# Kernel tuning notes

Hardware: AMD Instinct MI355X
Metric: run time of the kernel (lower is better)

Reference implementation:

```python
import jax, jax.numpy as jnp
import numpy as np

B, C, H, E, K, QT = 256, 1024, 64, 64, 2, 20000

def _mlp(x, W1, b1, W2, b2):
    # GKT MLP (eval mode: dropout off; batch-norm omitted, see notes)
    return jax.nn.relu(jax.nn.relu(x @ W1 + b1) @ W2 + b2)

def setup_inputs() -> dict:
    key = jax.random.key(0)
    ks = jax.random.split(key, 30)
    s = 0.05  # weight scale to keep pre-clamp activations in a sane range
    xt = jax.random.uniform(ks[0], (B,), dtype=jnp.float32)
    qt = jax.random.randint(ks[1], (B,), 0, QT)
    ht = jax.random.normal(ks[2], (B, C, H), dtype=jnp.float32)
    # binary question->concept incidence, ~4 KCs per question, col 0 forced on
    oh = (jax.random.uniform(ks[3], (QT, C)) < 4.0 / C).astype(jnp.float32)
    oh = oh.at[:, 0].set(1.0)
    qt_kc_one_hot = jnp.concatenate([oh, jnp.zeros((1, C), jnp.float32)], axis=0)  # zero padding row
    kc_embeddings = jax.random.normal(ks[4], (C, E), dtype=jnp.float32) * 0.1
    graphs = jax.random.uniform(ks[5], (K, C, C), dtype=jnp.float32)  # graph_model output
    neigh_weight = jnp.float32(0.8)
    MI = H + E
    Ws1 = jax.random.normal(ks[6], (MI, H), jnp.float32) * s; bs1 = jnp.zeros((H,), jnp.float32)
    Ws2 = jax.random.normal(ks[7], (H, H), jnp.float32) * s;  bs2 = jnp.zeros((H,), jnp.float32)
    Wn1 = jax.random.normal(ks[8], (K, 2 * MI, H), jnp.float32) * s; bn1 = jnp.zeros((K, H), jnp.float32)
    Wn2 = jax.random.normal(ks[9], (K, H, H), jnp.float32) * s;      bn2 = jnp.zeros((K, H), jnp.float32)
    ea_w = jax.random.uniform(ks[10], (C,), dtype=jnp.float32)
    We = jax.random.normal(ks[11], (H, H), jnp.float32) * s; be = jnp.zeros((H,), jnp.float32)
    Wa = jax.random.normal(ks[12], (H, H), jnp.float32) * s; ba = jnp.zeros((H,), jnp.float32)
    W_ih = jax.random.normal(ks[13], (H, 3 * H), jnp.float32) * s; b_ih = jnp.zeros((3 * H,), jnp.float32)
    W_hh = jax.random.normal(ks[14], (H, 3 * H), jnp.float32) * s; b_hh = jnp.zeros((3 * H,), jnp.float32)
    Wp = jax.random.normal(ks[15], (H, 1), jnp.float32) * s; bp = jnp.zeros((1,), jnp.float32)
    return dict(xt=xt, qt=qt, ht=ht, qt_kc_one_hot=qt_kc_one_hot, kc_embeddings=kc_embeddings,
                graphs=graphs, neigh_weight=neigh_weight, Ws1=Ws1, bs1=bs1, Ws2=Ws2, bs2=bs2,
                Wn1=Wn1, bn1=bn1, Wn2=Wn2, bn2=bn2, ea_w=ea_w, We=We, be=be, Wa=Wa, ba=ba,
                W_ih=W_ih, b_ih=b_ih, W_hh=W_hh, b_hh=b_hh, Wp=Wp, bp=bp)

def reference(xt, qt, ht, qt_kc_one_hot, kc_embeddings, graphs, neigh_weight,
              Ws1, bs1, Ws2, bs2, Wn1, bn1, Wn2, bn2, ea_w, We, be, Wa, ba,
              W_ih, b_ih, W_hh, b_hh, Wp, bp):
    # ---- _aggregate: the fusion loops never write back, so tmp_ht = cat(ht, kc_emb)
    mask = qt_kc_one_hot[qt]                                   # [B, C] gather of binary incidence
    kc = jnp.broadcast_to(kc_embeddings[None], (mask.shape[0], C, E))
    tmp_ht = jnp.concatenate([ht, kc], axis=-1)                # [B, C, H+E]
    # ---- _agg_neighbors
    self_ht = tmp_ht * mask[..., None]
    self_feat = jnp.clip(_mlp(self_ht, Ws1, bs1, Ws2, bs2), -10.0, 10.0)
    neigh_ht = jnp.clip(jnp.concatenate([self_ht, tmp_ht], axis=-1), -5.0, 5.0)  # [B,C,2(H+E)]
    # bug-faithful adj: mean of graphs[k] rows over sample 0's active concepts
    a0 = mask[0]                                               # [C]
    denom = jnp.maximum(a0.sum(), 1.0)
    adj = jnp.clip(jnp.einsum('c,kcd->kd', a0, graphs) / denom, -5.0, 5.0)       # [K, C]
    nb = jax.vmap(lambda W1, b1, W2, b2: _mlp(neigh_ht, W1, b1, W2, b2))(Wn1, bn1, Wn2, bn2)
    nb = jnp.clip(nb, -5.0, 5.0)                               # [K, B, C, H]
    w = jnp.clip(neigh_weight, 0.1, 0.9)
    nf = jnp.clip(adj[0][None, :, None] * nb[0], -5.0, 5.0)
    for k in range(1, K):
        nf = jnp.clip(w * nf + (1.0 - w) * adj[k][None, :, None] * nb[k], -5.0, 5.0)
    m_next = jnp.clip(jnp.where(mask[..., None] > 0.5, self_feat, nf), -50.0, 50.0)
    # ---- erase-add gate
    g = ea_w[None, :, None]
    res = m_next - g * jax.nn.sigmoid(m_next @ We + be) * m_next + g * jnp.tanh(m_next @ Wa + ba)
    # ---- GRUCell over flattened (B*C) rows
    gi = res @ W_ih + b_ih
    gh = ht @ W_hh + b_hh
    ir, iz, in_ = jnp.split(gi, 3, axis=-1)
    hr, hz, hn = jnp.split(gh, 3, axis=-1)
    r = jax.nn.sigmoid(ir + hr)
    z = jax.nn.sigmoid(iz + hz)
    n = jnp.tanh(in_ + r * hn)
    h_next = (1.0 - z) * n + z * ht                            # [B, C, H]
    y = jax.nn.sigmoid(h_next @ Wp + bp)[..., 0]               # [B, C]
    return y
```

## Files before the change

### kernel.cpp

```cpp
#include <hip/hip_runtime.h>

#define DEVINL __device__ __forceinline__

typedef __bf16 bf16x8 __attribute__((ext_vector_type(8)));
typedef float  f32x4  __attribute__((ext_vector_type(4)));

static constexpr size_t kAdjOff  = 0;
static constexpr size_t kBiasOff = 8192;
static constexpr size_t kFragOff = 8192 + 786432;

static constexpr int FB_Wn1h0 = 0,  FB_Wn1h1 = 8,  FB_Wn2_0 = 16, FB_Wn2_1 = 24;
static constexpr int FB_Ws1h  = 32, FB_Ws2   = 40, FB_We    = 48, FB_Wa    = 56;
static constexpr int FB_Wih   = 64, FB_Whh   = 88;

DEVINL unsigned short bf16r(float f) {
  unsigned u = __builtin_bit_cast(unsigned, f);
  unsigned r = ((u >> 16) & 1u) + 0x7FFFu;
  return (unsigned short)((u + r) >> 16);
}
DEVINL float sigmoidf_(float x) { return __builtin_amdgcn_rcpf(1.f + __expf(-x)); }
DEVINL float tanhf_(float x)    { return 1.f - 2.f * __builtin_amdgcn_rcpf(1.f + __expf(2.f * x)); }

DEVINL void lds_fence() {
  __builtin_amdgcn_sched_barrier(0);
  __builtin_amdgcn_s_waitcnt(0xC07F);
  __builtin_amdgcn_sched_barrier(0);
}

DEVINL f32x4 mfma16(bf16x8 a, bf16x8 b, f32x4 c) {
  return __builtin_amdgcn_mfma_f32_16x16x32_bf16(a, b, c, 0, 0, 0);
}

DEVINL unsigned clip2_(unsigned x) {
  float lo = __builtin_bit_cast(float, x << 16);
  float hi = __builtin_bit_cast(float, x & 0xFFFF0000u);
  lo = fminf(fmaxf(lo, -5.f), 5.f);
  hi = fminf(fmaxf(hi, -5.f), 5.f);
  return (__builtin_bit_cast(unsigned, lo) >> 16) | (__builtin_bit_cast(unsigned, hi) & 0xFFFF0000u);
}
DEVINL bf16x8 clip5(bf16x8 a) {
  uint4 u = __builtin_bit_cast(uint4, a);
  u.x = clip2_(u.x); u.y = clip2_(u.y); u.z = clip2_(u.z); u.w = clip2_(u.w);
  return __builtin_bit_cast(bf16x8, u);
}

__global__ void prep_adj_kernel(const int* __restrict__ qt, const float* __restrict__ onehot,
                                const float* __restrict__ graphs, float* __restrict__ adjw) {
  __shared__ float a0[1024];
  __shared__ float s_denom;
  const int tid = threadIdx.x;
  const int k = blockIdx.x >> 2, chunk = blockIdx.x & 3;
  const int q0 = qt[0];
  for (int i = tid; i < 1024; i += 256) a0[i] = onehot[(size_t)q0 * 1024 + i];
  __syncthreads();
  if (tid < 64) {
    float s = 0.f;
#pragma unroll
    for (int i = 0; i < 16; i++) s += a0[tid * 16 + i];
#pragma unroll
    for (int off = 32; off >= 1; off >>= 1) s += __shfl_xor(s, off, 64);
    if (tid == 0) s_denom = fmaxf(s, 1.0f);
  }
  __syncthreads();
  const int d = chunk * 256 + tid;
  const float* G = graphs + (size_t)k * 1024 * 1024 + d;
  float sum = 0.f;
  for (int c = 0; c < 1024; c++) sum += a0[c] * G[(size_t)c * 1024];
  adjw[k * 1024 + d] = fminf(fmaxf(sum / s_denom, -5.f), 5.f);
}

__global__ void prep_bias_kernel(const float* __restrict__ kc, const float* __restrict__ Wn1,
                                 const float* __restrict__ bn1, const float* __restrict__ Ws1,
                                 const float* __restrict__ bs1, float* __restrict__ biasTab) {
  int gid = blockIdx.x * 256 + threadIdx.x;
  int j = gid & 63;
  int c = (gid >> 6) & 1023;
  int tab = gid >> 16;
  const float* kcr = kc + (size_t)c * 64;
  float s;
  if (tab < 2) {
    s = bn1[tab * 64 + j];
    const float* W = Wn1 + ((size_t)tab * 256 + 192) * 64 + j;
#pragma unroll 4
    for (int e = 0; e < 64; e++) s += fminf(fmaxf(kcr[e], -5.f), 5.f) * W[(size_t)e * 64];
  } else {
    s = bs1[j];
    const float* W = Ws1 + (size_t)64 * 64 + j;
#pragma unroll 4
    for (int e = 0; e < 64; e++) s += kcr[e] * W[(size_t)e * 64];
  }
  int c16 = c >> 4, rr = c & 3, qq = (c & 15) >> 2, nt = j >> 4;
  int lane = qq * 16 + (j & 15);
  biasTab[(size_t)((((c16 * 3 + tab) * 4 + nt) * 64 + lane)) * 4 + rr] = s;
}

__global__ void prep_wfrag_kernel(const float* __restrict__ Wn1, const float* __restrict__ Wn2,
                                  const float* __restrict__ Ws1, const float* __restrict__ Ws2,
                                  const float* __restrict__ We,  const float* __restrict__ Wa,
                                  const float* __restrict__ Wih, const float* __restrict__ Whh,
                                  uint4* __restrict__ wfrag) {
  const int bid = blockIdx.x, lane = threadIdx.x;
  int mat, ks, nt;
  if (bid < 64) { mat = bid >> 3; ks = (bid >> 2) & 1; nt = bid & 3; }
  else { int f2 = bid - 64; mat = 8 + f2 / 24; int f = f2 % 24; ks = f / 12; nt = f % 12; }
  const float* base = Wn1; int stride = 64;
  switch (mat) {
    case 0: base = Wn1 + (size_t)128 * 64; break;
    case 1: base = Wn1 + (size_t)(256 + 128) * 64; break;
    case 2: base = Wn2; break;
    case 3: base = Wn2 + (size_t)64 * 64; break;
    case 4: base = Ws1; break;
    case 5: base = Ws2; break;
    case 6: base = We; break;
    case 7: base = Wa; break;
    case 8: base = Wih; stride = 192; break;
    case 9: base = Whh; stride = 192; break;
  }
  const int qq = lane >> 4, col = nt * 16 + (lane & 15);
  union { unsigned short u[8]; uint4 v; } tmp;
#pragma unroll
  for (int jj = 0; jj < 8; jj++) {
    int k = ks * 32 + qq * 8 + jj;
    tmp.u[jj] = bf16r(base[(size_t)k * stride + col]);
  }
  wfrag[(size_t)bid * 64 + lane] = tmp.v;
}

__global__ __launch_bounds__(256, 2) void gkt_main_kernel(
    const int* __restrict__ qt, const float* __restrict__ onehot, const float* __restrict__ ht,
    const float* __restrict__ nw, const float* __restrict__ bn2, const float* __restrict__ be,
    const float* __restrict__ ba, const float* __restrict__ bih, const float* __restrict__ bhh,
    const float* __restrict__ Wp, const float* __restrict__ bp, const float* __restrict__ eaw,
    const float* __restrict__ bs2, const float* __restrict__ adjw, const float* __restrict__ biasTab,
    const bf16x8* __restrict__ wfrag, float* __restrict__ out) {
  __shared__ __align__(16) unsigned short xbuf[4][32][72];
  __shared__ __align__(16) unsigned short hbuf[4][32][72];
  __shared__ float tokp[4][128];

  const int tid = threadIdx.x;
  const int wv = tid >> 6, lane = tid & 63;
  const int q = lane >> 4, cl = lane & 15;
  const int t0 = (blockIdx.x * 4 + wv) * 32;
  const int b = t0 >> 10, c0 = t0 & 1023, c16 = c0 >> 4;

  unsigned short* xb = &xbuf[wv][0][0];
  unsigned short* hb = &hbuf[wv][0][0];
  float* tp = &tokp[wv][0];

  if (lane < 32) {
    const int c = c0 + lane;
    tp[lane]      = onehot[(size_t)qt[b] * 1024 + c];
    tp[32 + lane] = adjw[c];
    tp[64 + lane] = adjw[1024 + c];
    tp[96 + lane] = eaw[c];
  }
  {
    const float4* ht4 = (const float4*)ht;
#pragma unroll
    for (int i = 0; i < 8; i++) {
      float4 v = ht4[(size_t)t0 * 16 + i * 64 + lane];
      int e = i * 64 + lane;
      int tok = e >> 4, coll = (e & 15) * 4;
      ushort4 h;
      h.x = bf16r(v.x); h.y = bf16r(v.y); h.z = bf16r(v.z); h.w = bf16r(v.w);
      *(ushort4*)&xbuf[wv][tok][coll] = h;
    }
  }
  lds_fence();

  const float wmix = fminf(fmaxf(nw[0], 0.1f), 0.9f);
  float wp4[4];
#pragma unroll
  for (int nt = 0; nt < 4; nt++) wp4[nt] = Wp[nt * 16 + cl];
  const float bpv = bp[0];

  auto ldA = [&](const unsigned short* buf, int mt, int ks) -> bf16x8 {
    return *(const bf16x8*)(buf + (cl + 16 * mt) * 72 + ks * 32 + q * 8);
  };
  auto ldB = [&](int frag) -> bf16x8 { return wfrag[frag * 64 + lane]; };
  const f32x4* bt4 = (const f32x4*)biasTab;

  bf16x8 xc[2][2];
#pragma unroll
  for (int mt = 0; mt < 2; mt++)
#pragma unroll
    for (int ks = 0; ks < 2; ks++) xc[mt][ks] = clip5(ldA(xb, mt, ks));

  f32x4 nf[2][4];
#pragma unroll
  for (int k2 = 0; k2 < 2; k2++) {
    f32x4 acc[2][4];
#pragma unroll
    for (int mt = 0; mt < 2; mt++)
#pragma unroll
      for (int nt = 0; nt < 4; nt++)
        acc[mt][nt] = bt4[(((c16 + mt) * 3 + k2) * 4 + nt) * 64 + lane];
#pragma unroll
    for (int ks = 0; ks < 2; ks++)
#pragma unroll
      for (int nt = 0; nt < 4; nt++) {
        bf16x8 bb = ldB((k2 ? FB_Wn1h1 : FB_Wn1h0) + ks * 4 + nt);
        acc[0][nt] = mfma16(xc[0][ks], bb, acc[0][nt]);
        acc[1][nt] = mfma16(xc[1][ks], bb, acc[1][nt]);
      }
    lds_fence();
#pragma unroll
    for (int mt = 0; mt < 2; mt++)
#pragma unroll
      for (int nt = 0; nt < 4; nt++)
#pragma unroll
        for (int r = 0; r < 4; r++)
          hb[(16 * mt + q * 4 + r) * 72 + nt * 16 + cl] = bf16r(fmaxf(acc[mt][nt][r], 0.f));
    lds_fence();
    f32x4 acc2[2][4];
#pragma unroll
    for (int nt = 0; nt < 4; nt++) {
      float bz = bn2[k2 * 64 + nt * 16 + cl];
      f32x4 iv = {bz, bz, bz, bz};
      acc2[0][nt] = iv; acc2[1][nt] = iv;
    }
#pragma unroll
    for (int ks = 0; ks < 2; ks++) {
      bf16x8 a0 = ldA(hb, 0, ks), a1 = ldA(hb, 1, ks);
#pragma unroll
      for (int nt = 0; nt < 4; nt++) {
        bf16x8 bb = ldB((k2 ? FB_Wn2_1 : FB_Wn2_0) + ks * 4 + nt);
        acc2[0][nt] = mfma16(a0, bb, acc2[0][nt]);
        acc2[1][nt] = mfma16(a1, bb, acc2[1][nt]);
      }
    }
#pragma unroll
    for (int mt = 0; mt < 2; mt++)
#pragma unroll
      for (int nt = 0; nt < 4; nt++)
#pragma unroll
        for (int r = 0; r < 4; r++) {
          int tok = 16 * mt + q * 4 + r;
          float nb = fminf(fmaxf(acc2[mt][nt][r], 0.f), 5.f);
          float v = tp[(1 + k2) * 32 + tok] * nb;
          if (k2 == 0) nf[mt][nt][r] = wmix * fminf(fmaxf(v, -5.f), 5.f);
          else         nf[mt][nt][r] = fminf(fmaxf(nf[mt][nt][r] + (1.f - wmix) * v, -5.f), 5.f);
        }
  }

  bool anySelf = __any((lane < 32) && (tp[lane] > 0.5f));
  if (anySelf) {
    bf16x8 xr[2][2];
#pragma unroll
    for (int mt = 0; mt < 2; mt++)
#pragma unroll
      for (int ks = 0; ks < 2; ks++) xr[mt][ks] = ldA(xb, mt, ks);
    f32x4 acc[2][4];
#pragma unroll
    for (int mt = 0; mt < 2; mt++)
#pragma unroll
      for (int nt = 0; nt < 4; nt++)
        acc[mt][nt] = bt4[(((c16 + mt) * 3 + 2) * 4 + nt) * 64 + lane];
#pragma unroll
    for (int ks = 0; ks < 2; ks++)
#pragma unroll
      for (int nt = 0; nt < 4; nt++) {
        bf16x8 bb = ldB(FB_Ws1h + ks * 4 + nt);
        acc[0][nt] = mfma16(xr[0][ks], bb, acc[0][nt]);
        acc[1][nt] = mfma16(xr[1][ks], bb, acc[1][nt]);
      }
    lds_fence();
#pragma unroll
    for (int mt = 0; mt < 2; mt++)
#pragma unroll
      for (int nt = 0; nt < 4; nt++)
#pragma unroll
        for (int r = 0; r < 4; r++)
          hb[(16 * mt + q * 4 + r) * 72 + nt * 16 + cl] = bf16r(fmaxf(acc[mt][nt][r], 0.f));
    lds_fence();
    f32x4 acc2[2][4];
#pragma unroll
    for (int nt = 0; nt < 4; nt++) {
      float bz = bs2[nt * 16 + cl];
      f32x4 iv = {bz, bz, bz, bz};
      acc2[0][nt] = iv; acc2[1][nt] = iv;
    }
#pragma unroll
    for (int ks = 0; ks < 2; ks++) {
      bf16x8 a0 = ldA(hb, 0, ks), a1 = ldA(hb, 1, ks);
#pragma unroll
      for (int nt = 0; nt < 4; nt++) {
        bf16x8 bb = ldB(FB_Ws2 + ks * 4 + nt);
        acc2[0][nt] = mfma16(a0, bb, acc2[0][nt]);
        acc2[1][nt] = mfma16(a1, bb, acc2[1][nt]);
      }
    }
#pragma unroll
    for (int mt = 0; mt < 2; mt++)
#pragma unroll
      for (int nt = 0; nt < 4; nt++)
#pragma unroll
        for (int r = 0; r < 4; r++) {
          int tok = 16 * mt + q * 4 + r;
          float sf = fminf(fmaxf(acc2[mt][nt][r], 0.f), 10.f);
          nf[mt][nt][r] = (tp[tok] > 0.5f) ? sf : nf[mt][nt][r];
        }
  }

  lds_fence();
#pragma unroll
  for (int mt = 0; mt < 2; mt++)
#pragma unroll
    for (int nt = 0; nt < 4; nt++)
#pragma unroll
      for (int r = 0; r < 4; r++)
        hb[(16 * mt + q * 4 + r) * 72 + nt * 16 + cl] = bf16r(nf[mt][nt][r]);
  lds_fence();
  bf16x8 mf[2][2];
#pragma unroll
  for (int mt = 0; mt < 2; mt++)
#pragma unroll
    for (int ks = 0; ks < 2; ks++) mf[mt][ks] = ldA(hb, mt, ks);
  {
    f32x4 accE[2][4];
#pragma unroll
    for (int nt = 0; nt < 4; nt++) {
      float bz = be[nt * 16 + cl];
      f32x4 iv = {bz, bz, bz, bz};
      accE[0][nt] = iv; accE[1][nt] = iv;
    }
#pragma unroll
    for (int ks = 0; ks < 2; ks++)
#pragma unroll
      for (int nt = 0; nt < 4; nt++) {
        bf16x8 bb = ldB(FB_We + ks * 4 + nt);
        accE[0][nt] = mfma16(mf[0][ks], bb, accE[0][nt]);
        accE[1][nt] = mfma16(mf[1][ks], bb, accE[1][nt]);
      }
#pragma unroll
    for (int mt = 0; mt < 2; mt++)
#pragma unroll
      for (int nt = 0; nt < 4; nt++)
#pragma unroll
        for (int r = 0; r < 4; r++) {
          int tok = 16 * mt + q * 4 + r;
          float g = tp[96 + tok];
          float m = nf[mt][nt][r];
          nf[mt][nt][r] = m - g * sigmoidf_(accE[mt][nt][r]) * m;
        }
    f32x4 accA[2][4];
#pragma unroll
    for (int nt = 0; nt < 4; nt++) {
      float bz = ba[nt * 16 + cl];
      f32x4 iv = {bz, bz, bz, bz};
      accA[0][nt] = iv; accA[1][nt] = iv;
    }
#pragma unroll
    for (int ks = 0; ks < 2; ks++)
#pragma unroll
      for (int nt = 0; nt < 4; nt++) {
        bf16x8 bb = ldB(FB_Wa + ks * 4 + nt);
        accA[0][nt] = mfma16(mf[0][ks], bb, accA[0][nt]);
        accA[1][nt] = mfma16(mf[1][ks], bb, accA[1][nt]);
      }
#pragma unroll
    for (int mt = 0; mt < 2; mt++)
#pragma unroll
      for (int nt = 0; nt < 4; nt++)
#pragma unroll
        for (int r = 0; r < 4; r++) {
          int tok = 16 * mt + q * 4 + r;
          nf[mt][nt][r] += tp[96 + tok] * tanhf_(accA[mt][nt][r]);
        }
  }

  lds_fence();
#pragma unroll
  for (int mt = 0; mt < 2; mt++)
#pragma unroll
    for (int nt = 0; nt < 4; nt++)
#pragma unroll
      for (int r = 0; r < 4; r++)
        hb[(16 * mt + q * 4 + r) * 72 + nt * 16 + cl] = bf16r(nf[mt][nt][r]);
  lds_fence();
  bf16x8 rf[2][2], xr2[2][2];
#pragma unroll
  for (int mt = 0; mt < 2; mt++)
#pragma unroll
    for (int ks = 0; ks < 2; ks++) { rf[mt][ks] = ldA(hb, mt, ks); xr2[mt][ks] = ldA(xb, mt, ks); }

  f32x4 gR[2][4], gZ[2][4], gN[2][4], gH[2][4];
#pragma unroll
  for (int nt = 0; nt < 4; nt++) {
    int col = nt * 16 + cl;
    float brz = bih[col] + bhh[col];
    float bzz = bih[64 + col] + bhh[64 + col];
    float bnn = bih[128 + col];
    float bhn = bhh[128 + col];
    f32x4 v;
    v = {brz, brz, brz, brz}; gR[0][nt] = v; gR[1][nt] = v;
    v = {bzz, bzz, bzz, bzz}; gZ[0][nt] = v; gZ[1][nt] = v;
    v = {bnn, bnn, bnn, bnn}; gN[0][nt] = v; gN[1][nt] = v;
    v = {bhn, bhn, bhn, bhn}; gH[0][nt] = v; gH[1][nt] = v;
  }
#pragma unroll
  for (int ks = 0; ks < 2; ks++)
#pragma unroll
    for (int nt = 0; nt < 4; nt++) {
      bf16x8 bi_r = ldB(FB_Wih + ks * 12 + nt);
      bf16x8 bh_r = ldB(FB_Whh + ks * 12 + nt);
      bf16x8 bi_z = ldB(FB_Wih + ks * 12 + 4 + nt);
      bf16x8 bh_z = ldB(FB_Whh + ks * 12 + 4 + nt);
      bf16x8 bi_n = ldB(FB_Wih + ks * 12 + 8 + nt);
      bf16x8 bh_n = ldB(FB_Whh + ks * 12 + 8 + nt);
#pragma unroll
      for (int mt = 0; mt < 2; mt++) {
        gR[mt][nt] = mfma16(rf[mt][ks],  bi_r, gR[mt][nt]);
        gR[mt][nt] = mfma16(xr2[mt][ks], bh_r, gR[mt][nt]);
        gZ[mt][nt] = mfma16(rf[mt][ks],  bi_z, gZ[mt][nt]);
        gZ[mt][nt] = mfma16(xr2[mt][ks], bh_z, gZ[mt][nt]);
        gN[mt][nt] = mfma16(rf[mt][ks],  bi_n, gN[mt][nt]);
        gH[mt][nt] = mfma16(xr2[mt][ks], bh_n, gH[mt][nt]);
      }
    }
#pragma unroll
  for (int mt = 0; mt < 2; mt++)
#pragma unroll
    for (int nt = 0; nt < 4; nt++)
#pragma unroll
      for (int r = 0; r < 4; r++) {
        gR[mt][nt][r] = sigmoidf_(gR[mt][nt][r]);
        gZ[mt][nt][r] = sigmoidf_(gZ[mt][nt][r]);
      }

#pragma unroll
  for (int mt = 0; mt < 2; mt++)
#pragma unroll
    for (int r = 0; r < 4; r++) {
      int tok = 16 * mt + q * 4 + r;
      float part = 0.f;
#pragma unroll
      for (int nt = 0; nt < 4; nt++) {
        float nval = tanhf_(gN[mt][nt][r] + gR[mt][nt][r] * gH[mt][nt][r]);
        float z = gZ[mt][nt][r];
        float htv = ht[(size_t)(t0 + tok) * 64 + nt * 16 + cl];
        float hnx = (1.f - z) * nval + z * htv;
        part += hnx * wp4[nt];
      }
      part += __shfl_xor(part, 1, 64);
      part += __shfl_xor(part, 2, 64);
      part += __shfl_xor(part, 4, 64);
      part += __shfl_xor(part, 8, 64);
      if (cl == 0) out[t0 + tok] = sigmoidf_(part + bpv);
    }
}

extern "C" void kernel_launch(void* const* d_in, const int* in_sizes, int n_in,
                              void* d_out, int out_size, void* d_ws, size_t ws_size,
                              hipStream_t stream) {
  const int*   qt     = (const int*)d_in[1];
  const float* ht     = (const float*)d_in[2];
  const float* onehot = (const float*)d_in[3];
  const float* kc     = (const float*)d_in[4];
  const float* graphs = (const float*)d_in[5];
  const float* nw     = (const float*)d_in[6];
  const float* Ws1    = (const float*)d_in[7];
  const float* bs1    = (const float*)d_in[8];
  const float* Ws2    = (const float*)d_in[9];
  const float* bs2    = (const float*)d_in[10];
  const float* Wn1    = (const float*)d_in[11];
  const float* bn1    = (const float*)d_in[12];
  const float* Wn2    = (const float*)d_in[13];
  const float* bn2    = (const float*)d_in[14];
  const float* eaw    = (const float*)d_in[15];
  const float* We     = (const float*)d_in[16];
  const float* be     = (const float*)d_in[17];
  const float* Wa     = (const float*)d_in[18];
  const float* ba     = (const float*)d_in[19];
  const float* Wih    = (const float*)d_in[20];
  const float* bih    = (const float*)d_in[21];
  const float* Whh    = (const float*)d_in[22];
  const float* bhh    = (const float*)d_in[23];
  const float* Wp     = (const float*)d_in[24];
  const float* bp     = (const float*)d_in[25];
  float* out = (float*)d_out;

  float* adjw    = (float*)((char*)d_ws + kAdjOff);
  float* biasTab = (float*)((char*)d_ws + kBiasOff);
  uint4* wfragU  = (uint4*)((char*)d_ws + kFragOff);

  prep_adj_kernel<<<8, 256, 0, stream>>>(qt, onehot, graphs, adjw);
  prep_bias_kernel<<<768, 256, 0, stream>>>(kc, Wn1, bn1, Ws1, bs1, biasTab);
  prep_wfrag_kernel<<<112, 64, 0, stream>>>(Wn1, Wn2, Ws1, Ws2, We, Wa, Wih, Whh, wfragU);
  gkt_main_kernel<<<2048, 256, 0, stream>>>(qt, onehot, ht, nw, bn2, be, ba, bih, bhh,
                                            Wp, bp, eaw, bs2, adjw, biasTab,
                                            (const bf16x8*)wfragU, out);
}
```

Baseline: 314.4 us.

## Drop xbuf LDS, keep ht in registers, raise occupancy, sparsify adj prep

The main kernel stops keeping a separate LDS buffer for ht. It loads the ht fragments once into registers and reuses them for the self-MLP and the GRU hidden matmul. The freed LDS and the launch bounds raised to 4 blocks per CU aim at higher occupancy, and the per-token scalars are now read as vector loads. The adjacency prep now gathers only the nonzero one-hot entries (about 4 of 1024), which removes nearly all of its strided graph reads. The risks are register spilling under the tighter occupancy target and extra live registers for xr.

```diff
diff --git a/kernel.cpp b/kernel.cpp
--- a/kernel.cpp
+++ b/kernel.cpp
@@ -46,27 +46,34 @@
 
 __global__ void prep_adj_kernel(const int* __restrict__ qt, const float* __restrict__ onehot,
                                 const float* __restrict__ graphs, float* __restrict__ adjw) {
-  __shared__ float a0[1024];
-  __shared__ float s_denom;
+  __shared__ float a0v[1024];
+  __shared__ int   aidx[1024];
+  __shared__ int   s_nnz;
+  __shared__ float s_den;
   const int tid = threadIdx.x;
   const int k = blockIdx.x >> 2, chunk = blockIdx.x & 3;
+  if (tid == 0) { s_nnz = 0; s_den = 0.f; }
+  __syncthreads();
   const int q0 = qt[0];
-  for (int i = tid; i < 1024; i += 256) a0[i] = onehot[(size_t)q0 * 1024 + i];
+  float lsum = 0.f;
+#pragma unroll
+  for (int i = 0; i < 4; i++) {
+    int c = tid * 4 + i;
+    float v = onehot[(size_t)q0 * 1024 + c];
+    lsum += v;
+    if (v != 0.f) { int p = atomicAdd(&s_nnz, 1); aidx[p] = c; a0v[p] = v; }
+  }
+#pragma unroll
+  for (int off = 32; off >= 1; off >>= 1) lsum += __shfl_xor(lsum, off, 64);
+  if ((tid & 63) == 0) atomicAdd(&s_den, lsum);
   __syncthreads();
-  if (tid < 64) {
-    float s = 0.f;
-#pragma unroll
-    for (int i = 0; i < 16; i++) s += a0[tid * 16 + i];
-#pragma unroll
-    for (int off = 32; off >= 1; off >>= 1) s += __shfl_xor(s, off, 64);
-    if (tid == 0) s_denom = fmaxf(s, 1.0f);
-  }
-  __syncthreads();
+  const float denom = fmaxf(s_den, 1.f);
+  const int nnz = s_nnz;
   const int d = chunk * 256 + tid;
-  const float* G = graphs + (size_t)k * 1024 * 1024 + d;
+  const float* G = graphs + (size_t)k * 1048576 + d;
   float sum = 0.f;
-  for (int c = 0; c < 1024; c++) sum += a0[c] * G[(size_t)c * 1024];
-  adjw[k * 1024 + d] = fminf(fmaxf(sum / s_denom, -5.f), 5.f);
+  for (int j = 0; j < nnz; j++) sum += a0v[j] * G[(size_t)aidx[j] * 1024];
+  adjw[k * 1024 + d] = fminf(fmaxf(sum / denom, -5.f), 5.f);
 }
 
 __global__ void prep_bias_kernel(const float* __restrict__ kc, const float* __restrict__ Wn1,
@@ -126,16 +133,15 @@
   wfrag[(size_t)bid * 64 + lane] = tmp.v;
 }
 
-__global__ __launch_bounds__(256, 2) void gkt_main_kernel(
+__global__ __launch_bounds__(256, 4) void gkt_main_kernel(
     const int* __restrict__ qt, const float* __restrict__ onehot, const float* __restrict__ ht,
     const float* __restrict__ nw, const float* __restrict__ bn2, const float* __restrict__ be,
     const float* __restrict__ ba, const float* __restrict__ bih, const float* __restrict__ bhh,
     const float* __restrict__ Wp, const float* __restrict__ bp, const float* __restrict__ eaw,
     const float* __restrict__ bs2, const float* __restrict__ adjw, const float* __restrict__ biasTab,
     const bf16x8* __restrict__ wfrag, float* __restrict__ out) {
-  __shared__ __align__(16) unsigned short xbuf[4][32][72];
   __shared__ __align__(16) unsigned short hbuf[4][32][72];
-  __shared__ float tokp[4][128];
+  __shared__ __align__(16) float tokp[4][128];
 
   const int tid = threadIdx.x;
   const int wv = tid >> 6, lane = tid & 63;
@@ -143,7 +149,6 @@
   const int t0 = (blockIdx.x * 4 + wv) * 32;
   const int b = t0 >> 10, c0 = t0 & 1023, c16 = c0 >> 4;
 
-  unsigned short* xb = &xbuf[wv][0][0];
   unsigned short* hb = &hbuf[wv][0][0];
   float* tp = &tokp[wv][0];
 
@@ -163,7 +168,7 @@
       int tok = e >> 4, coll = (e & 15) * 4;
       ushort4 h;
       h.x = bf16r(v.x); h.y = bf16r(v.y); h.z = bf16r(v.z); h.w = bf16r(v.w);
-      *(ushort4*)&xbuf[wv][tok][coll] = h;
+      *(ushort4*)&hbuf[wv][tok][coll] = h;
     }
   }
   lds_fence();
@@ -174,36 +179,104 @@
   for (int nt = 0; nt < 4; nt++) wp4[nt] = Wp[nt * 16 + cl];
   const float bpv = bp[0];
 
-  auto ldA = [&](const unsigned short* buf, int mt, int ks) -> bf16x8 {
-    return *(const bf16x8*)(buf + (cl + 16 * mt) * 72 + ks * 32 + q * 8);
+  auto ldA = [&](int mt, int ks) -> bf16x8 {
+    return *(const bf16x8*)(hb + (cl + 16 * mt) * 72 + ks * 32 + q * 8);
   };
   auto ldB = [&](int frag) -> bf16x8 { return wfrag[frag * 64 + lane]; };
+  auto ldTP4 = [&](int base, int mt) -> f32x4 {
+    return *(const f32x4*)(tp + base + 16 * mt + q * 4);
+  };
   const f32x4* bt4 = (const f32x4*)biasTab;
 
-  bf16x8 xc[2][2];
-#pragma unroll
-  for (int mt = 0; mt < 2; mt++)
-#pragma unroll
-    for (int ks = 0; ks < 2; ks++) xc[mt][ks] = clip5(ldA(xb, mt, ks));
+  bf16x8 xr[2][2];
+#pragma unroll
+  for (int mt = 0; mt < 2; mt++)
+#pragma unroll
+    for (int ks = 0; ks < 2; ks++) xr[mt][ks] = ldA(mt, ks);
+  lds_fence();
 
   f32x4 nf[2][4];
-#pragma unroll
-  for (int k2 = 0; k2 < 2; k2++) {
+  {
+    bf16x8 xc[2][2];
+#pragma unroll
+    for (int mt = 0; mt < 2; mt++)
+#pragma unroll
+      for (int ks = 0; ks < 2; ks++) xc[mt][ks] = clip5(xr[mt][ks]);
+
+#pragma unroll
+    for (int k2 = 0; k2 < 2; k2++) {
+      f32x4 acc[2][4];
+#pragma unroll
+      for (int mt = 0; mt < 2; mt++)
+#pragma unroll
+        for (int nt = 0; nt < 4; nt++)
+          acc[mt][nt] = bt4[(((c16 + mt) * 3 + k2) * 4 + nt) * 64 + lane];
+#pragma unroll
+      for (int ks = 0; ks < 2; ks++)
+#pragma unroll
+        for (int nt = 0; nt < 4; nt++) {
+          bf16x8 bb = ldB((k2 ? FB_Wn1h1 : FB_Wn1h0) + ks * 4 + nt);
+          acc[0][nt] = mfma16(xc[0][ks], bb, acc[0][nt]);
+          acc[1][nt] = mfma16(xc[1][ks], bb, acc[1][nt]);
+        }
+#pragma unroll
+      for (int mt = 0; mt < 2; mt++)
+#pragma unroll
+        for (int nt = 0; nt < 4; nt++)
+#pragma unroll
+          for (int r = 0; r < 4; r++)
+            hb[(16 * mt + q * 4 + r) * 72 + nt * 16 + cl] = bf16r(fmaxf(acc[mt][nt][r], 0.f));
+      lds_fence();
+      f32x4 acc2[2][4];
+#pragma unroll
+      for (int nt = 0; nt < 4; nt++) {
+        float bz = bn2[k2 * 64 + nt * 16 + cl];
+        f32x4 iv = {bz, bz, bz, bz};
+        acc2[0][nt] = iv; acc2[1][nt] = iv;
+      }
+#pragma unroll
+      for (int ks = 0; ks < 2; ks++) {
+        bf16x8 a0 = ldA(0, ks), a1 = ldA(1, ks);
+#pragma unroll
+        for (int nt = 0; nt < 4; nt++) {
+          bf16x8 bb = ldB((k2 ? FB_Wn2_1 : FB_Wn2_0) + ks * 4 + nt);
+          acc2[0][nt] = mfma16(a0, bb, acc2[0][nt]);
+          acc2[1][nt] = mfma16(a1, bb, acc2[1][nt]);
+        }
+      }
+      lds_fence();
+#pragma unroll
+      for (int mt = 0; mt < 2; mt++) {
+        f32x4 adjv = ldTP4((1 + k2) * 32, mt);
+#pragma unroll
+        for (int nt = 0; nt < 4; nt++)
+#pragma unroll
+          for (int r = 0; r < 4; r++) {
+            float nb = fminf(fmaxf(acc2[mt][nt][r], 0.f), 5.f);
+            float v = adjv[r] * nb;
+            if (k2 == 0) nf[mt][nt][r] = wmix * fminf(fmaxf(v, -5.f), 5.f);
+            else         nf[mt][nt][r] = fminf(fmaxf(nf[mt][nt][r] + (1.f - wmix) * v, -5.f), 5.f);
+          }
+      }
+    }
+  }
+
+  bool anySelf = __any((lane < 32) && (tp[lane] > 0.5f));
+  if (anySelf) {
     f32x4 acc[2][4];
 #pragma unroll
     for (int mt = 0; mt < 2; mt++)
 #pragma unroll
       for (int nt = 0; nt < 4; nt++)
-        acc[mt][nt] = bt4[(((c16 + mt) * 3 + k2) * 4 + nt) * 64 + lane];
+        acc[mt][nt] = bt4[(((c16 + mt) * 3 + 2) * 4 + nt) * 64 + lane];
 #pragma unroll
     for (int ks = 0; ks < 2; ks++)
 #pragma unroll
       for (int nt = 0; nt < 4; nt++) {
-        bf16x8 bb = ldB((k2 ? FB_Wn1h1 : FB_Wn1h0) + ks * 4 + nt);
-        acc[0][nt] = mfma16(xc[0][ks], bb, acc[0][nt]);
-        acc[1][nt] = mfma16(xc[1][ks], bb, acc[1][nt]);
-      }
-    lds_fence();
+        bf16x8 bb = ldB(FB_Ws1h + ks * 4 + nt);
+        acc[0][nt] = mfma16(xr[0][ks], bb, acc[0][nt]);
+        acc[1][nt] = mfma16(xr[1][ks], bb, acc[1][nt]);
+      }
 #pragma unroll
     for (int mt = 0; mt < 2; mt++)
 #pragma unroll
@@ -215,74 +288,13 @@
     f32x4 acc2[2][4];
 #pragma unroll
     for (int nt = 0; nt < 4; nt++) {
-      float bz = bn2[k2 * 64 + nt * 16 + cl];
-      f32x4 iv = {bz, bz, bz, bz};
-      acc2[0][nt] = iv; acc2[1][nt] = iv;
-    }
-#pragma unroll
-    for (int ks = 0; ks < 2; ks++) {
-      bf16x8 a0 = ldA(hb, 0, ks), a1 = ldA(hb, 1, ks);
-#pragma unroll
-      for (int nt = 0; nt < 4; nt++) {
-        bf16x8 bb = ldB((k2 ? FB_Wn2_1 : FB_Wn2_0) + ks * 4 + nt);
-        acc2[0][nt] = mfma16(a0, bb, acc2[0][nt]);
-        acc2[1][nt] = mfma16(a1, bb, acc2[1][nt]);
-      }
-    }
-#pragma unroll
-    for (int mt = 0; mt < 2; mt++)
-#pragma unroll
-      for (int nt = 0; nt < 4; nt++)
-#pragma unroll
-        for (int r = 0; r < 4; r++) {
-          int tok = 16 * mt + q * 4 + r;
-          float nb = fminf(fmaxf(acc2[mt][nt][r], 0.f), 5.f);
-          float v = tp[(1 + k2) * 32 + tok] * nb;
-          if (k2 == 0) nf[mt][nt][r] = wmix * fminf(fmaxf(v, -5.f), 5.f);
-          else         nf[mt][nt][r] = fminf(fmaxf(nf[mt][nt][r] + (1.f - wmix) * v, -5.f), 5.f);
-        }
-  }
-
-  bool anySelf = __any((lane < 32) && (tp[lane] > 0.5f));
-  if (anySelf) {
-    bf16x8 xr[2][2];
-#pragma unroll
-    for (int mt = 0; mt < 2; mt++)
-#pragma unroll
-      for (int ks = 0; ks < 2; ks++) xr[mt][ks] = ldA(xb, mt, ks);
-    f32x4 acc[2][4];
-#pragma unroll
-    for (int mt = 0; mt < 2; mt++)
-#pragma unroll
-      for (int nt = 0; nt < 4; nt++)
-        acc[mt][nt] = bt4[(((c16 + mt) * 3 + 2) * 4 + nt) * 64 + lane];
-#pragma unroll
-    for (int ks = 0; ks < 2; ks++)
-#pragma unroll
-      for (int nt = 0; nt < 4; nt++) {
-        bf16x8 bb = ldB(FB_Ws1h + ks * 4 + nt);
-        acc[0][nt] = mfma16(xr[0][ks], bb, acc[0][nt]);
-        acc[1][nt] = mfma16(xr[1][ks], bb, acc[1][nt]);
-      }
-    lds_fence();
-#pragma unroll
-    for (int mt = 0; mt < 2; mt++)
-#pragma unroll
-      for (int nt = 0; nt < 4; nt++)
-#pragma unroll
-        for (int r = 0; r < 4; r++)
-          hb[(16 * mt + q * 4 + r) * 72 + nt * 16 + cl] = bf16r(fmaxf(acc[mt][nt][r], 0.f));
-    lds_fence();
-    f32x4 acc2[2][4];
-#pragma unroll
-    for (int nt = 0; nt < 4; nt++) {
       float bz = bs2[nt * 16 + cl];
       f32x4 iv = {bz, bz, bz, bz};
       acc2[0][nt] = iv; acc2[1][nt] = iv;
     }
 #pragma unroll
     for (int ks = 0; ks < 2; ks++) {
-      bf16x8 a0 = ldA(hb, 0, ks), a1 = ldA(hb, 1, ks);
+      bf16x8 a0 = ldA(0, ks), a1 = ldA(1, ks);
 #pragma unroll
       for (int nt = 0; nt < 4; nt++) {
         bf16x8 bb = ldB(FB_Ws2 + ks * 4 + nt);
@@ -290,19 +302,20 @@
         acc2[1][nt] = mfma16(a1, bb, acc2[1][nt]);
       }
     }
-#pragma unroll
-    for (int mt = 0; mt < 2; mt++)
+    lds_fence();
+#pragma unroll
+    for (int mt = 0; mt < 2; mt++) {
+      f32x4 mk = ldTP4(0, mt);
 #pragma unroll
       for (int nt = 0; nt < 4; nt++)
 #pragma unroll
         for (int r = 0; r < 4; r++) {
-          int tok = 16 * mt + q * 4 + r;
           float sf = fminf(fmaxf(acc2[mt][nt][r], 0.f), 10.f);
-          nf[mt][nt][r] = (tp[tok] > 0.5f) ? sf : nf[mt][nt][r];
+          nf[mt][nt][r] = (mk[r] > 0.5f) ? sf : nf[mt][nt][r];
         }
-  }
-
-  lds_fence();
+    }
+  }
+
 #pragma unroll
   for (int mt = 0; mt < 2; mt++)
 #pragma unroll
@@ -315,7 +328,8 @@
 #pragma unroll
   for (int mt = 0; mt < 2; mt++)
 #pragma unroll
-    for (int ks = 0; ks < 2; ks++) mf[mt][ks] = ldA(hb, mt, ks);
+    for (int ks = 0; ks < 2; ks++) mf[mt][ks] = ldA(mt, ks);
+  lds_fence();
   {
     f32x4 accE[2][4];
 #pragma unroll
@@ -333,16 +347,16 @@
         accE[1][nt] = mfma16(mf[1][ks], bb, accE[1][nt]);
       }
 #pragma unroll
-    for (int mt = 0; mt < 2; mt++)
+    for (int mt = 0; mt < 2; mt++) {
+      f32x4 gv = ldTP4(96, mt);
 #pragma unroll
       for (int nt = 0; nt < 4; nt++)
 #pragma unroll
         for (int r = 0; r < 4; r++) {
-          int tok = 16 * mt + q * 4 + r;
-          float g = tp[96 + tok];
           float m = nf[mt][nt][r];
-          nf[mt][nt][r] = m - g * sigmoidf_(accE[mt][nt][r]) * m;
+          nf[mt][nt][r] = m - gv[r] * sigmoidf_(accE[mt][nt][r]) * m;
         }
+    }
     f32x4 accA[2][4];
 #pragma unroll
     for (int nt = 0; nt < 4; nt++) {
@@ -359,17 +373,16 @@
         accA[1][nt] = mfma16(mf[1][ks], bb, accA[1][nt]);
       }
 #pragma unroll
-    for (int mt = 0; mt < 2; mt++)
+    for (int mt = 0; mt < 2; mt++) {
+      f32x4 gv = ldTP4(96, mt);
 #pragma unroll
       for (int nt = 0; nt < 4; nt++)
 #pragma unroll
-        for (int r = 0; r < 4; r++) {
-          int tok = 16 * mt + q * 4 + r;
-          nf[mt][nt][r] += tp[96 + tok] * tanhf_(accA[mt][nt][r]);
-        }
-  }
-
-  lds_fence();
+        for (int r = 0; r < 4; r++)
+          nf[mt][nt][r] += gv[r] * tanhf_(accA[mt][nt][r]);
+    }
+  }
+
 #pragma unroll
   for (int mt = 0; mt < 2; mt++)
 #pragma unroll
@@ -378,11 +391,11 @@
       for (int r = 0; r < 4; r++)
         hb[(16 * mt + q * 4 + r) * 72 + nt * 16 + cl] = bf16r(nf[mt][nt][r]);
   lds_fence();
-  bf16x8 rf[2][2], xr2[2][2];
-#pragma unroll
-  for (int mt = 0; mt < 2; mt++)
-#pragma unroll
-    for (int ks = 0; ks < 2; ks++) { rf[mt][ks] = ldA(hb, mt, ks); xr2[mt][ks] = ldA(xb, mt, ks); }
+  bf16x8 rf[2][2];
+#pragma unroll
+  for (int mt = 0; mt < 2; mt++)
+#pragma unroll
+    for (int ks = 0; ks < 2; ks++) rf[mt][ks] = ldA(mt, ks);
 
   f32x4 gR[2][4], gZ[2][4], gN[2][4], gH[2][4];
 #pragma unroll
@@ -410,23 +423,14 @@
       bf16x8 bh_n = ldB(FB_Whh + ks * 12 + 8 + nt);
 #pragma unroll
       for (int mt = 0; mt < 2; mt++) {
-        gR[mt][nt] = mfma16(rf[mt][ks],  bi_r, gR[mt][nt]);
-        gR[mt][nt] = mfma16(xr2[mt][ks], bh_r, gR[mt][nt]);
-        gZ[mt][nt] = mfma16(rf[mt][ks],  bi_z, gZ[mt][nt]);
-        gZ[mt][nt] = mfma16(xr2[mt][ks], bh_z, gZ[mt][nt]);
-        gN[mt][nt] = mfma16(rf[mt][ks],  bi_n, gN[mt][nt]);
-        gH[mt][nt] = mfma16(xr2[mt][ks], bh_n, gH[mt][nt]);
-      }
-    }
-#pragma unroll
-  for (int mt = 0; mt < 2; mt++)
-#pragma unroll
-    for (int nt = 0; nt < 4; nt++)
-#pragma unroll
-      for (int r = 0; r < 4; r++) {
-        gR[mt][nt][r] = sigmoidf_(gR[mt][nt][r]);
-        gZ[mt][nt][r] = sigmoidf_(gZ[mt][nt][r]);
-      }
+        gR[mt][nt] = mfma16(rf[mt][ks], bi_r, gR[mt][nt]);
+        gR[mt][nt] = mfma16(xr[mt][ks], bh_r, gR[mt][nt]);
+        gZ[mt][nt] = mfma16(rf[mt][ks], bi_z, gZ[mt][nt]);
+        gZ[mt][nt] = mfma16(xr[mt][ks], bh_z, gZ[mt][nt]);
+        gN[mt][nt] = mfma16(rf[mt][ks], bi_n, gN[mt][nt]);
+        gH[mt][nt] = mfma16(xr[mt][ks], bh_n, gH[mt][nt]);
+      }
+    }
 
 #pragma unroll
   for (int mt = 0; mt < 2; mt++)
@@ -436,10 +440,11 @@
       float part = 0.f;
 #pragma unroll
       for (int nt = 0; nt < 4; nt++) {
-        float nval = tanhf_(gN[mt][nt][r] + gR[mt][nt][r] * gH[mt][nt][r]);
-        float z = gZ[mt][nt][r];
+        float rr = sigmoidf_(gR[mt][nt][r]);
+        float zz = sigmoidf_(gZ[mt][nt][r]);
+        float nval = tanhf_(gN[mt][nt][r] + rr * gH[mt][nt][r]);
         float htv = ht[(size_t)(t0 + tok) * 64 + nt * 16 + cl];
-        float hnx = (1.f - z) * nval + z * htv;
+        float hnx = (1.f - zz) * nval + zz * htv;
         part += hnx * wp4[nt];
       }
       part += __shfl_xor(part, 1, 64);
```

Result: slower. 345.0 us (+9.7%).
